# Optimization experiments

Hardware: AMD Instinct MI355X
Metric: run time of the kernel (lower is better)

## Reference

```python
import jax, jax.numpy as jnp
import numpy as np

HIDDEN = 2048
N_LAYERS = 2
CHOICE_NUM = 19  # (task_num-1)*2 + 1 with task_num=10, adapt=False
VOCAB = CHOICE_NUM + 1


def setup_inputs() -> dict:
    key = jax.random.key(0)
    ks = jax.random.split(key, 16)
    s = 0.02
    inp = {}
    inp["input_idx"] = jax.random.randint(ks[0], (1,), 0, VOCAB)
    inp["task"] = 5  # python int; 1+task <= CHOICE_NUM
    inp["embedding"] = jax.random.normal(ks[1], (VOCAB, HIDDEN), dtype=jnp.float32) * s
    k = 2
    for i in range(N_LAYERS):
        inp[f"w_ih_{i}"] = jax.random.normal(ks[k + 0], (4 * HIDDEN, HIDDEN), dtype=jnp.float32) * s
        inp[f"w_hh_{i}"] = jax.random.normal(ks[k + 1], (4 * HIDDEN, HIDDEN), dtype=jnp.float32) * s
        inp[f"b_ih_{i}"] = jax.random.normal(ks[k + 2], (4 * HIDDEN,), dtype=jnp.float32) * s
        inp[f"b_hh_{i}"] = jax.random.normal(ks[k + 3], (4 * HIDDEN,), dtype=jnp.float32) * s
        k += 4
    inp["w_choice"] = jax.random.normal(ks[k], (CHOICE_NUM, HIDDEN), dtype=jnp.float32) * s
    inp["b_choice"] = jax.random.normal(ks[k + 1], (CHOICE_NUM,), dtype=jnp.float32) * s
    return inp


def _lstm_cell(x, h, c, w_ih, w_hh, b_ih, b_hh):
    # x, h, c: [1, H]; torch LSTMCell gate order: i, f, g, o
    gates = x @ w_ih.T + b_ih + h @ w_hh.T + b_hh  # [1, 4H]
    i, f, g, o = jnp.split(gates, 4, axis=-1)
    c_next = jax.nn.sigmoid(f) * c + jax.nn.sigmoid(i) * jnp.tanh(g)
    h_next = jax.nn.sigmoid(o) * jnp.tanh(c_next)
    return h_next, c_next


def reference(input_idx, task, embedding,
              w_ih_0, w_hh_0, b_ih_0, b_hh_0,
              w_ih_1, w_hh_1, b_ih_1, b_hh_1,
              w_choice, b_choice):
    x = embedding[input_idx].reshape(1, -1)  # [1, H]
    layers = [(w_ih_0, w_hh_0, b_ih_0, b_hh_0),
              (w_ih_1, w_hh_1, b_ih_1, b_hh_1)]
    zeros = jnp.zeros((1, HIDDEN), dtype=x.dtype)
    for (w_ih, w_hh, b_ih, b_hh) in layers:
        # hidden=None in the torch module -> per-layer zero initial state
        h, c = _lstm_cell(x, zeros, zeros, w_ih, w_hh, b_ih, b_hh)
        x = h
    logit = (x @ w_choice.T + b_choice).reshape(-1)  # [CHOICE_NUM]
    mask = jnp.arange(CHOICE_NUM) < (1 + task)  # adapt=False: prefix 1+task ones
    logit = jnp.where(mask, logit, jnp.float32(-1e9))
    return logit
```

## Files before the change

### kernel.cpp

```cpp
#include <hip/hip_runtime.h>

#define HIDDEN 2048
#define CHOICE_NUM 19

__global__ __launch_bounds__(192) void lstm_layer_kernel(
    const float* __restrict__ w_ih,
    const float* __restrict__ b_ih,
    const float* __restrict__ b_hh,
    const float* __restrict__ x_base,
    const int* __restrict__ idx_ptr,
    float* __restrict__ h_out)
{
    const int unit = blockIdx.x;
    const int wave = threadIdx.x >> 6;
    const int lane = threadIdx.x & 63;

    const int gate_off = (wave == 0) ? 0 : (wave == 1 ? 2 * HIDDEN : 3 * HIDDEN);
    const int row = gate_off + unit;

    const float* x = x_base + (idx_ptr ? (size_t)idx_ptr[0] * HIDDEN : 0);
    const float4* wrow = (const float4*)(w_ih + (size_t)row * HIDDEN);
    const float4* xv   = (const float4*)x;

    float sum = 0.f;
    #pragma unroll
    for (int j = 0; j < 8; ++j) {
        int k = lane + j * 64;
        float4 wv = wrow[k];
        float4 xx = xv[k];
        sum += wv.x * xx.x + wv.y * xx.y + wv.z * xx.z + wv.w * xx.w;
    }
    #pragma unroll
    for (int off = 32; off; off >>= 1)
        sum += __shfl_down(sum, off, 64);

    __shared__ float g_lds[3];
    if (lane == 0) g_lds[wave] = sum + b_ih[row] + b_hh[row];
    __syncthreads();
    if (threadIdx.x == 0) {
        float gi = g_lds[0], gg = g_lds[1], go = g_lds[2];
        float si = 1.f / (1.f + expf(-gi));
        float so = 1.f / (1.f + expf(-go));
        float c  = si * tanhf(gg);
        h_out[unit] = so * tanhf(c);
    }
}

__global__ __launch_bounds__(256) void logits_kernel(
    const float* __restrict__ w_choice,
    const float* __restrict__ b_choice,
    const float* __restrict__ h,
    const int* __restrict__ task_ptr,
    float* __restrict__ out)
{
    const int r = blockIdx.x;
    const int t = threadIdx.x;
    const float4* wrow = (const float4*)(w_choice + (size_t)r * HIDDEN);
    const float4* xv   = (const float4*)h;

    float sum = 0.f;
    #pragma unroll
    for (int j = 0; j < 2; ++j) {
        int k = t + j * 256;
        float4 wv = wrow[k];
        float4 xx = xv[k];
        sum += wv.x * xx.x + wv.y * xx.y + wv.z * xx.z + wv.w * xx.w;
    }
    #pragma unroll
    for (int off = 32; off; off >>= 1)
        sum += __shfl_down(sum, off, 64);

    __shared__ float partial[4];
    if ((t & 63) == 0) partial[t >> 6] = sum;
    __syncthreads();
    if (t == 0) {
        float v = partial[0] + partial[1] + partial[2] + partial[3] + b_choice[r];
        int task = task_ptr[0];
        out[r] = (r < 1 + task) ? v : -1e9f;
    }
}

extern "C" void kernel_launch(void* const* d_in, const int* in_sizes, int n_in,
                              void* d_out, int out_size, void* d_ws, size_t ws_size,
                              hipStream_t stream) {
    const int*   input_idx = (const int*)d_in[0];
    const int*   task      = (const int*)d_in[1];
    const float* emb       = (const float*)d_in[2];
    const float* w_ih0     = (const float*)d_in[3];
    const float* b_ih0     = (const float*)d_in[5];
    const float* b_hh0     = (const float*)d_in[6];
    const float* w_ih1     = (const float*)d_in[7];
    const float* b_ih1     = (const float*)d_in[9];
    const float* b_hh1     = (const float*)d_in[10];
    const float* w_choice  = (const float*)d_in[11];
    const float* b_choice  = (const float*)d_in[12];

    float* h0 = (float*)d_ws;
    float* h1 = h0 + HIDDEN;

    lstm_layer_kernel<<<HIDDEN, 192, 0, stream>>>(w_ih0, b_ih0, b_hh0, emb, input_idx, h0);
    lstm_layer_kernel<<<HIDDEN, 192, 0, stream>>>(w_ih1, b_ih1, b_hh1, h0, nullptr, h1);
    logits_kernel<<<CHOICE_NUM, 256, 0, stream>>>(w_choice, b_choice, h1, task, (float*)d_out);
}
```

Measured before the change: 25.80 us.

## Fuse LSTM layers and logits into one cooperative kernel with weight prefetch

Replaces the three launches with a single cooperative kernel that uses grid-wide syncs between layer 0, layer 1 and the logits. Before the first sync, each wave prefetches its first layer-1 weight rows into registers, so that load overlaps with the layer-0 compute. The aim is to cut launch overhead and hide layer-1 weight latency. In exchange it pays for grid.sync and makes host-side occupancy queries on every call, and it falls back to the old three-kernel path if the cooperative launch fails. The fallback logits kernel is also shrunk to one wave per row.

```diff
diff --git a/kernel.cpp b/kernel.cpp
--- a/kernel.cpp
+++ b/kernel.cpp
@@ -1,104 +1,190 @@
 #include <hip/hip_runtime.h>
+#include <hip/hip_cooperative_groups.h>
 
-#define HIDDEN 2048
-#define CHOICE_NUM 19
+namespace cg = cooperative_groups;
+
+#define H 2048
+#define CH 19
+
+__device__ __forceinline__ float wred(float s) {
+    #pragma unroll
+    for (int off = 32; off; off >>= 1) s += __shfl_down(s, off, 64);
+    return s;
+}
+
+__device__ __forceinline__ float dot_row(const float4* __restrict__ row,
+                                         const float4* __restrict__ x, int lane) {
+    float s = 0.f;
+    #pragma unroll
+    for (int j = 0; j < 8; ++j) {
+        float4 w = row[lane + j * 64];
+        float4 v = x[lane + j * 64];
+        s += w.x * v.x + w.y * v.y + w.z * v.z + w.w * v.w;
+    }
+    return s;
+}
+
+__global__ __launch_bounds__(256, 2) void fused_kernel(
+    const int* __restrict__ idxp, const int* __restrict__ taskp,
+    const float* __restrict__ emb,
+    const float* __restrict__ w0, const float* __restrict__ bi0, const float* __restrict__ bh0,
+    const float* __restrict__ w1, const float* __restrict__ bi1, const float* __restrict__ bh1,
+    const float* __restrict__ wc, const float* __restrict__ bc,
+    float* __restrict__ out, float* __restrict__ ws)
+{
+    cg::grid_group grid = cg::this_grid();
+    const int lane = threadIdx.x & 63;
+    const int gw   = blockIdx.x * 4 + (threadIdx.x >> 6);
+    const int W    = gridDim.x * 4;
+    float* h0 = ws;
+    float* h1 = ws + H;
+
+    const float4* xv = (const float4*)(emb + (size_t)idxp[0] * H);
+
+    const int u0 = gw;
+    float4 p_i[8], p_g[8], p_o[8];
+    {
+        const float4* a = (const float4*)(w1 + (size_t)u0 * H);
+        const float4* b = (const float4*)(w1 + (size_t)(2 * H + u0) * H);
+        const float4* c = (const float4*)(w1 + (size_t)(3 * H + u0) * H);
+        #pragma unroll
+        for (int j = 0; j < 8; ++j) p_i[j] = a[lane + j * 64];
+        #pragma unroll
+        for (int j = 0; j < 8; ++j) p_g[j] = b[lane + j * 64];
+        #pragma unroll
+        for (int j = 0; j < 8; ++j) p_o[j] = c[lane + j * 64];
+    }
+
+    for (int u = gw; u < H; u += W) {
+        float ai = wred(dot_row((const float4*)(w0 + (size_t)u * H),           xv, lane));
+        float ag = wred(dot_row((const float4*)(w0 + (size_t)(2 * H + u) * H), xv, lane));
+        float ao = wred(dot_row((const float4*)(w0 + (size_t)(3 * H + u) * H), xv, lane));
+        if (lane == 0) {
+            float gi = ai + bi0[u]         + bh0[u];
+            float gg = ag + bi0[2 * H + u] + bh0[2 * H + u];
+            float go = ao + bi0[3 * H + u] + bh0[3 * H + u];
+            float si  = 1.f / (1.f + expf(-gi));
+            float so_ = 1.f / (1.f + expf(-go));
+            h0[u] = so_ * tanhf(si * tanhf(gg));
+        }
+    }
+    grid.sync();
+
+    const float4* h0v = (const float4*)h0;
+    for (int u = gw; u < H; u += W) {
+        float ai, ag, ao;
+        if (u == u0) {
+            ai = ag = ao = 0.f;
+            #pragma unroll
+            for (int j = 0; j < 8; ++j) {
+                float4 hv = h0v[lane + j * 64];
+                ai += p_i[j].x * hv.x + p_i[j].y * hv.y + p_i[j].z * hv.z + p_i[j].w * hv.w;
+                ag += p_g[j].x * hv.x + p_g[j].y * hv.y + p_g[j].z * hv.z + p_g[j].w * hv.w;
+                ao += p_o[j].x * hv.x + p_o[j].y * hv.y + p_o[j].z * hv.z + p_o[j].w * hv.w;
+            }
+        } else {
+            ai = dot_row((const float4*)(w1 + (size_t)u * H),           h0v, lane);
+            ag = dot_row((const float4*)(w1 + (size_t)(2 * H + u) * H), h0v, lane);
+            ao = dot_row((const float4*)(w1 + (size_t)(3 * H + u) * H), h0v, lane);
+        }
+        ai = wred(ai); ag = wred(ag); ao = wred(ao);
+        if (lane == 0) {
+            float gi = ai + bi1[u]         + bh1[u];
+            float gg = ag + bi1[2 * H + u] + bh1[2 * H + u];
+            float go = ao + bi1[3 * H + u] + bh1[3 * H + u];
+            float si  = 1.f / (1.f + expf(-gi));
+            float so_ = 1.f / (1.f + expf(-go));
+            h1[u] = so_ * tanhf(si * tanhf(gg));
+        }
+    }
+    grid.sync();
+
+    const float4* h1v = (const float4*)h1;
+    for (int r = gw; r < CH; r += W) {
+        float s = wred(dot_row((const float4*)(wc + (size_t)r * H), h1v, lane));
+        if (lane == 0) {
+            int task = taskp[0];
+            out[r] = (r < 1 + task) ? (s + bc[r]) : -1e9f;
+        }
+    }
+}
 
 __global__ __launch_bounds__(192) void lstm_layer_kernel(
-    const float* __restrict__ w_ih,
-    const float* __restrict__ b_ih,
-    const float* __restrict__ b_hh,
-    const float* __restrict__ x_base,
-    const int* __restrict__ idx_ptr,
-    float* __restrict__ h_out)
+    const float* __restrict__ w_ih, const float* __restrict__ b_ih,
+    const float* __restrict__ b_hh, const float* __restrict__ x_base,
+    const int* __restrict__ idx_ptr, float* __restrict__ h_out)
 {
     const int unit = blockIdx.x;
     const int wave = threadIdx.x >> 6;
     const int lane = threadIdx.x & 63;
-
-    const int gate_off = (wave == 0) ? 0 : (wave == 1 ? 2 * HIDDEN : 3 * HIDDEN);
+    const int gate_off = (wave == 0) ? 0 : (wave == 1 ? 2 * H : 3 * H);
     const int row = gate_off + unit;
-
-    const float* x = x_base + (idx_ptr ? (size_t)idx_ptr[0] * HIDDEN : 0);
-    const float4* wrow = (const float4*)(w_ih + (size_t)row * HIDDEN);
-    const float4* xv   = (const float4*)x;
-
-    float sum = 0.f;
-    #pragma unroll
-    for (int j = 0; j < 8; ++j) {
-        int k = lane + j * 64;
-        float4 wv = wrow[k];
-        float4 xx = xv[k];
-        sum += wv.x * xx.x + wv.y * xx.y + wv.z * xx.z + wv.w * xx.w;
-    }
-    #pragma unroll
-    for (int off = 32; off; off >>= 1)
-        sum += __shfl_down(sum, off, 64);
-
+    const float* x = x_base + (idx_ptr ? (size_t)idx_ptr[0] * H : 0);
+    float sum = wred(dot_row((const float4*)(w_ih + (size_t)row * H), (const float4*)x, lane));
     __shared__ float g_lds[3];
     if (lane == 0) g_lds[wave] = sum + b_ih[row] + b_hh[row];
     __syncthreads();
     if (threadIdx.x == 0) {
-        float gi = g_lds[0], gg = g_lds[1], go = g_lds[2];
-        float si = 1.f / (1.f + expf(-gi));
-        float so = 1.f / (1.f + expf(-go));
-        float c  = si * tanhf(gg);
-        h_out[unit] = so * tanhf(c);
+        float si = 1.f / (1.f + expf(-g_lds[0]));
+        float so = 1.f / (1.f + expf(-g_lds[2]));
+        h_out[unit] = so * tanhf(si * tanhf(g_lds[1]));
     }
 }
 
-__global__ __launch_bounds__(256) void logits_kernel(
-    const float* __restrict__ w_choice,
-    const float* __restrict__ b_choice,
-    const float* __restrict__ h,
-    const int* __restrict__ task_ptr,
+__global__ __launch_bounds__(64) void logits_kernel(
+    const float* __restrict__ wc, const float* __restrict__ bc,
+    const float* __restrict__ h, const int* __restrict__ taskp,
     float* __restrict__ out)
 {
     const int r = blockIdx.x;
-    const int t = threadIdx.x;
-    const float4* wrow = (const float4*)(w_choice + (size_t)r * HIDDEN);
-    const float4* xv   = (const float4*)h;
-
-    float sum = 0.f;
-    #pragma unroll
-    for (int j = 0; j < 2; ++j) {
-        int k = t + j * 256;
-        float4 wv = wrow[k];
-        float4 xx = xv[k];
-        sum += wv.x * xx.x + wv.y * xx.y + wv.z * xx.z + wv.w * xx.w;
-    }
-    #pragma unroll
-    for (int off = 32; off; off >>= 1)
-        sum += __shfl_down(sum, off, 64);
-
-    __shared__ float partial[4];
-    if ((t & 63) == 0) partial[t >> 6] = sum;
-    __syncthreads();
-    if (t == 0) {
-        float v = partial[0] + partial[1] + partial[2] + partial[3] + b_choice[r];
-        int task = task_ptr[0];
-        out[r] = (r < 1 + task) ? v : -1e9f;
+    const int lane = threadIdx.x;
+    float s = wred(dot_row((const float4*)(wc + (size_t)r * H), (const float4*)h, lane));
+    if (lane == 0) {
+        int task = taskp[0];
+        out[r] = (r < 1 + task) ? (s + bc[r]) : -1e9f;
     }
 }
 
 extern "C" void kernel_launch(void* const* d_in, const int* in_sizes, int n_in,
                               void* d_out, int out_size, void* d_ws, size_t ws_size,
                               hipStream_t stream) {
-    const int*   input_idx = (const int*)d_in[0];
-    const int*   task      = (const int*)d_in[1];
-    const float* emb       = (const float*)d_in[2];
-    const float* w_ih0     = (const float*)d_in[3];
-    const float* b_ih0     = (const float*)d_in[5];
-    const float* b_hh0     = (const float*)d_in[6];
-    const float* w_ih1     = (const float*)d_in[7];
-    const float* b_ih1     = (const float*)d_in[9];
-    const float* b_hh1     = (const float*)d_in[10];
-    const float* w_choice  = (const float*)d_in[11];
-    const float* b_choice  = (const float*)d_in[12];
+    const int*   idx  = (const int*)d_in[0];
+    const int*   task = (const int*)d_in[1];
+    const float* emb  = (const float*)d_in[2];
+    const float* w0   = (const float*)d_in[3];
+    const float* bi0  = (const float*)d_in[5];
+    const float* bh0  = (const float*)d_in[6];
+    const float* w1   = (const float*)d_in[7];
+    const float* bi1  = (const float*)d_in[9];
+    const float* bh1  = (const float*)d_in[10];
+    const float* wc   = (const float*)d_in[11];
+    const float* bc   = (const float*)d_in[12];
+    float* out = (float*)d_out;
+    float* ws  = (float*)d_ws;
 
-    float* h0 = (float*)d_ws;
-    float* h1 = h0 + HIDDEN;
+    int dev = 0;
+    (void)hipGetDevice(&dev);
+    int numCU = 0;
+    (void)hipDeviceGetAttribute(&numCU, hipDeviceAttributeMultiprocessorCount, dev);
+    int occ = 0;
+    hipError_t oe = hipOccupancyMaxActiveBlocksPerMultiprocessor(&occ, fused_kernel, 256, 0);
 
-    lstm_layer_kernel<<<HIDDEN, 192, 0, stream>>>(w_ih0, b_ih0, b_hh0, emb, input_idx, h0);
-    lstm_layer_kernel<<<HIDDEN, 192, 0, stream>>>(w_ih1, b_ih1, b_hh1, h0, nullptr, h1);
-    logits_kernel<<<CHOICE_NUM, 256, 0, stream>>>(w_choice, b_choice, h1, task, (float*)d_out);
+    int maxBlocks = (oe == hipSuccess && numCU > 0) ? occ * numCU : 0;
+    int gridBlocks = maxBlocks < 512 ? maxBlocks : 512;
+
+    if (gridBlocks >= 128) {
+        void* args[] = {(void*)&idx, (void*)&task, (void*)&emb,
+                        (void*)&w0, (void*)&bi0, (void*)&bh0,
+                        (void*)&w1, (void*)&bi1, (void*)&bh1,
+                        (void*)&wc, (void*)&bc, (void*)&out, (void*)&ws};
+        hipError_t le = hipLaunchCooperativeKernel(fused_kernel, dim3(gridBlocks),
+                                                   dim3(256), args, 0, stream);
+        if (le == hipSuccess) return;
+    }
+
+    float* h0 = ws;
+    float* h1 = ws + H;
+    lstm_layer_kernel<<<H, 192, 0, stream>>>(w0, bi0, bh0, emb, idx, h0);
+    lstm_layer_kernel<<<H, 192, 0, stream>>>(w1, bi1, bh1, h0, nullptr, h1);
+    logits_kernel<<<CH, 64, 0, stream>>>(wc, bc, h1, task, out);
 }
```

Result: slower. 90.04 us (+249.0%).
